# Performance work log

Measured on AMD Instinct MI355X. Metric: run time of the kernel, lower is better.

## Reference

```python
import jax, jax.numpy as jnp
import numpy as np

D_CONV = 4
DT_RANK = 64
D_STATE = 16

def silu(v):
    return v * jax.nn.sigmoid(v)

def setup_inputs() -> dict:
    key = jax.random.key(0)
    ks = jax.random.split(key, 10)
    B, L, d_model, d_inner = 2, 2048, 1024, 2048
    def nrm(k, shape, scale):
        return jax.random.normal(k, shape, dtype=jnp.float32) * scale
    A = jnp.tile(jnp.arange(1, D_STATE + 1, dtype=jnp.float32), (d_inner, 1))
    return {
        'x': nrm(ks[0], (B, L, d_model), 1.0),
        'W_in': nrm(ks[1], (d_model, 2 * d_inner), d_model ** -0.5),
        'conv_w': nrm(ks[2], (d_inner, D_CONV), D_CONV ** -0.5),
        'conv_b': nrm(ks[3], (d_inner,), 0.02),
        'W_x': nrm(ks[4], (d_inner, DT_RANK + 2 * D_STATE), d_inner ** -0.5),
        'W_dt': nrm(ks[5], (DT_RANK, d_inner), DT_RANK ** -0.5),
        'b_dt': nrm(ks[6], (d_inner,), 0.02),
        'A_log': jnp.log(A),
        'D': jnp.ones((d_inner,), dtype=jnp.float32),
        'W_out': nrm(ks[7], (d_inner, d_model), d_inner ** -0.5),
    }

def reference(x, W_in, conv_w, conv_b, W_x, W_dt, b_dt, A_log, D, W_out):
    B, L, _ = x.shape
    d_inner = W_dt.shape[1]
    # input projection and gate split
    xz = x @ W_in                                   # [B, L, 2*d_inner]
    xb, z = jnp.split(xz, 2, axis=-1)
    # causal depthwise conv1d (pad left d_conv-1, then first L outputs)
    xp = jnp.pad(xb, ((0, 0), (D_CONV - 1, 0), (0, 0)))
    xc = sum(xp[:, k:k + L, :] * conv_w[:, k] for k in range(D_CONV)) + conv_b
    xb = silu(xc)                                   # [B, L, d_inner]
    # data-dependent SSM parameters
    x_dbl = xb @ W_x                                # [B, L, dt_rank + 2*d_state]
    dt_low, Bm, Cm = jnp.split(x_dbl, [DT_RANK, DT_RANK + D_STATE], axis=-1)
    dt = jax.nn.softplus(dt_low @ W_dt + b_dt)      # [B, L, d_inner]
    A = -jnp.exp(A_log)                             # [d_inner, d_state]

    def step(h, inp):
        dt_t, B_t, C_t, x_t = inp                   # [B,d_inner],[B,n],[B,n],[B,d_inner]
        dA = jnp.exp(A * dt_t[..., None])           # [B, d_inner, d_state]
        h = h * dA + (x_t * dt_t)[..., None] * B_t[:, None, :]
        y = jnp.einsum('bdn,bn->bd', h, C_t)
        return h, y

    xs = (dt.swapaxes(0, 1), Bm.swapaxes(0, 1), Cm.swapaxes(0, 1), xb.swapaxes(0, 1))
    h0 = jnp.zeros((B, d_inner, D_STATE), dtype=x.dtype)
    _, ys = jax.lax.scan(step, h0, xs)              # ys: [L, B, d_inner]
    y = ys.swapaxes(0, 1) + xb * D
    out = y * silu(z)
    return out @ W_out
```

## Files before the change

kernel.cpp:

```cpp
#include <hip/hip_runtime.h>
#include <hip/hip_bf16.h>


#define BATCH   2
#define SEQLEN  2048
#define DMODEL  1024
#define DINNER  2048
#define DCONV   4
#define DTRANK  64
#define DSTATE  16
#define BL      (BATCH * SEQLEN)
#define NXZ     (2 * DINNER)
#define XDBL_N  (DTRANK + 2 * DSTATE)
#define LCH     32
#define NCHUNK  (SEQLEN / LCH)
#define KSPLIT  8
#define KC      (DINNER / KSPLIT)
#define KS_OUT  4
#define KCO     (DINNER / KS_OUT)
#define KS_XD   8
#define KCX     (DINNER / KS_XD)
#define XDP     128

typedef __bf16 bf16x8 __attribute__((ext_vector_type(8)));
typedef __bf16 bf16x4 __attribute__((ext_vector_type(4)));
typedef float  floatx4 __attribute__((ext_vector_type(4)));

__device__ __forceinline__ float silu_f(float v) {
    return v / (1.f + __expf(-v));
}

__device__ __forceinline__ float softplus_f(float v) {
    return (v > 20.f) ? v : __logf(1.f + __expf(v));
}

__device__ __forceinline__ float fast_exp2(float v) {
    return __builtin_amdgcn_exp2f(v);
}

__device__ __forceinline__ void gload_lds16(const __bf16* g, __bf16* l) {
    __builtin_amdgcn_global_load_lds(
        (const __attribute__((address_space(1))) void*)g,
        (__attribute__((address_space(3))) void*)l, 16, 0, 0);
}

#define VMW(n) asm volatile("s_waitcnt vmcnt(" #n ")" ::: "memory")
#define BARX() __builtin_amdgcn_s_barrier()

template <int BUF, int QA>
__device__ __forceinline__ void rdA(const char* rA, bf16x8 (&aF)[4][2]) {
#pragma unroll
    for (int j = 0; j < 4; ++j) {
        aF[j][0] = *(const bf16x8*)(rA + BUF * 65536 + ((QA * 4 + j) * 2 + 0) * 1024);
        aF[j][1] = *(const bf16x8*)(rA + BUF * 65536 + ((QA * 4 + j) * 2 + 1) * 1024);
    }
}

template <int BUF, int QB>
__device__ __forceinline__ void rdB(const char* rB, bf16x8 (&bF)[2][2]) {
#pragma unroll
    for (int f = 0; f < 2; ++f) {
        bF[f][0] = *(const bf16x8*)(rB + BUF * 65536 + QB * 8192 + f * 2048 + 0);
        bF[f][1] = *(const bf16x8*)(rB + BUF * 65536 + QB * 8192 + f * 2048 + 1024);
    }
}

template <int QA, int QB>
__device__ __forceinline__ void mf16(const bf16x8 (&aF)[4][2], const bf16x8 (&bF)[2][2],
                                     floatx4 (&acc)[8][4]) {
    __builtin_amdgcn_s_setprio(1);
#pragma unroll
    for (int ks = 0; ks < 2; ++ks)
#pragma unroll
        for (int j = 0; j < 4; ++j)
#pragma unroll
            for (int f = 0; f < 2; ++f)
                acc[QA * 4 + j][QB * 2 + f] = __builtin_amdgcn_mfma_f32_16x16x32_bf16(
                    aF[j][ks], bF[f][ks], acc[QA * 4 + j][QB * 2 + f], 0, 0, 0);
    __builtin_amdgcn_s_setprio(0);
}

template <int BUF, int QA>
__device__ __forceinline__ void stA2(const __bf16* gAs, char* sm, int lda, int w, int t) {
    gload_lds16(gAs + (size_t)(QA * 64) * lda + t * 64,
                (__bf16*)(sm + BUF * 65536 + QA * 8192 + w * 1024));
    gload_lds16(gAs + (size_t)(128 + QA * 64) * lda + t * 64,
                (__bf16*)(sm + BUF * 65536 + 16384 + QA * 8192 + w * 1024));
}

template <int BUF, int QB>
__device__ __forceinline__ void stB2(const __bf16* gBs, char* sm, int lda, int w, int t) {
    gload_lds16(gBs + (size_t)(QB * 32) * lda + t * 64,
                (__bf16*)(sm + BUF * 65536 + 32768 + QB * 8192 + w * 1024));
    gload_lds16(gBs + (size_t)(128 + QB * 32) * lda + t * 64,
                (__bf16*)(sm + BUF * 65536 + 32768 + 16384 + QB * 8192 + w * 1024));
}

template <int EPI>
__global__ __launch_bounds__(512, 2) void gemm_bt_256(
    const __bf16* __restrict__ A,
    const __bf16* __restrict__ BT,
    void* __restrict__ Cv,
    int M, int N, int K, int lda,
    const float* __restrict__ bias)
{
    __shared__ __align__(16) char smem[131072];

    const int tid  = threadIdx.x;
    const int w    = tid >> 6;
    const int lane = tid & 63;

    const int cpx = gridDim.x >> 3;
    const int swz = (blockIdx.x & 7) * cpx + (blockIdx.x >> 3);
    const int ntn = N >> 8;
    const int row0 = (swz / ntn) << 8;
    const int col0 = (swz % ntn) << 8;
    const int kbase = blockIdx.y * K;

    const int P     = tid;
    const int rr    = (P >> 2) & 15;
    const int qq    = (P & 3) ^ (2 * ((P >> 5) & 1));
    const int colE  = (((P >> 6) & 1) * 4 + qq) * 8;
    const int rgP   = P >> 7;
    const int rowAu = rgP * 16 + rr;
    const int rowBu = (rgP >> 1) * 64 + (rgP & 1) * 16 + rr;

    const __bf16* gAs = A  + (size_t)(row0 + rowAu) * lda + kbase + colE;
    const __bf16* gBs = BT + (size_t)(col0 + rowBu) * lda + kbase + colE;
    char* sm = smem;

    const int lsw = ((lane & 15) * 4 + ((lane >> 4) ^ (2 * ((lane >> 3) & 1)))) * 16;
    const char* rA = smem + (w >> 2) * 16384 + lsw;
    const char* rB = smem + 32768 + ((w & 3) >> 1) * 16384 + ((w & 3) & 1) * 4096 + lsw;

    floatx4 acc[8][4];
#pragma unroll
    for (int i = 0; i < 8; ++i)
#pragma unroll
        for (int j = 0; j < 4; ++j)
            acc[i][j] = (floatx4){0.f, 0.f, 0.f, 0.f};
    bf16x8 aF[4][2], bF[2][2];

    const int NT = K >> 6;
    const int NI = NT >> 1;

    stA2<0, 0>(gAs, sm, lda, w, 0);
    stB2<0, 0>(gBs, sm, lda, w, 0);
    stB2<0, 1>(gBs, sm, lda, w, 0);
    stA2<0, 1>(gAs, sm, lda, w, 0);
    stA2<1, 0>(gAs, sm, lda, w, 1);
    stB2<1, 1>(gBs, sm, lda, w, 1);
    VMW(6);
    BARX();

    for (int i = 0; i < NI - 1; ++i) {
        const int t1 = 2 * i + 1, t2 = 2 * i + 2, t3 = 2 * i + 3;
        rdA<0, 0>(rA, aF); rdB<0, 0>(rB, bF);
        stB2<1, 0>(gBs, sm, lda, w, t1);
        BARX(); mf16<0, 0>(aF, bF, acc); BARX();
        rdB<0, 1>(rB, bF);
        stA2<1, 1>(gAs, sm, lda, w, t1);
        BARX(); mf16<0, 1>(aF, bF, acc); VMW(8); BARX();
        rdA<0, 1>(rA, aF);
        stA2<0, 0>(gAs, sm, lda, w, t2);
        BARX(); mf16<1, 1>(aF, bF, acc); BARX();
        rdB<0, 0>(rB, bF);
        stB2<0, 1>(gBs, sm, lda, w, t2);
        BARX(); mf16<1, 0>(aF, bF, acc); VMW(6); BARX();
        rdA<1, 0>(rA, aF); rdB<1, 0>(rB, bF);
        stB2<0, 0>(gBs, sm, lda, w, t2);
        BARX(); mf16<0, 0>(aF, bF, acc); BARX();
        rdB<1, 1>(rB, bF);
        stA2<0, 1>(gAs, sm, lda, w, t2);
        BARX(); mf16<0, 1>(aF, bF, acc); VMW(8); BARX();
        rdA<1, 1>(rA, aF);
        stA2<1, 0>(gAs, sm, lda, w, t3);
        BARX(); mf16<1, 1>(aF, bF, acc); BARX();
        rdB<1, 0>(rB, bF);
        stB2<1, 1>(gBs, sm, lda, w, t3);
        BARX(); mf16<1, 0>(aF, bF, acc); VMW(6); BARX();
    }
    {
        const int t1 = NT - 1;
        rdA<0, 0>(rA, aF); rdB<0, 0>(rB, bF);
        stB2<1, 0>(gBs, sm, lda, w, t1);
        BARX(); mf16<0, 0>(aF, bF, acc); BARX();
        rdB<0, 1>(rB, bF);
        stA2<1, 1>(gAs, sm, lda, w, t1);
        BARX(); mf16<0, 1>(aF, bF, acc); VMW(8); BARX();
        rdA<0, 1>(rA, aF);
        BARX(); mf16<1, 1>(aF, bF, acc); BARX();
        rdB<0, 0>(rB, bF);
        BARX(); mf16<1, 0>(aF, bF, acc); VMW(2); BARX();
        rdA<1, 0>(rA, aF); rdB<1, 0>(rB, bF);
        BARX(); mf16<0, 0>(aF, bF, acc); BARX();
        rdB<1, 1>(rB, bF);
        BARX(); mf16<0, 1>(aF, bF, acc); VMW(0); BARX();
        rdA<1, 1>(rA, aF);
        BARX(); mf16<1, 1>(aF, bF, acc); BARX();
        rdB<1, 0>(rB, bF);
        BARX(); mf16<1, 0>(aF, bF, acc);
    }

    const int lrow = lane & 15, quad = lane >> 4;
    const int rbase = row0 + (w >> 2) * 128;
    const int cbase = col0 + (w & 3) * 64;
    const size_t cofs = (size_t)blockIdx.y * (size_t)M * (size_t)N;
#pragma unroll
    for (int fi = 0; fi < 8; ++fi) {
#pragma unroll
        for (int cf = 0; cf < 4; ++cf) {
            const int col = cbase + cf * 16 + lrow;
            const float bv = (EPI == 1 || EPI == 3) ? bias[col] : 0.f;
#pragma unroll
            for (int r = 0; r < 4; ++r) {
                const int row = rbase + fi * 16 + quad * 4 + r;
                float v = acc[fi][cf][r];
                if (EPI == 1 || EPI == 3) v = softplus_f(v + bv);
                if (EPI == 2 || EPI == 3)
                    ((__bf16*)Cv)[(size_t)row * N + col] = (__bf16)v;
                else
                    ((float*)Cv)[cofs + (size_t)row * N + col] = v;
            }
        }
    }
    (void)M;
}

__global__ __launch_bounds__(256) void out_reduce(
    const float* __restrict__ parts, float* __restrict__ out)
{
    const size_t i = ((size_t)blockIdx.x * 256 + threadIdx.x) * 4;
    floatx4 s = *(const floatx4*)(parts + i);
#pragma unroll
    for (int kz = 1; kz < KS_OUT; ++kz)
        s += *(const floatx4*)(parts + (size_t)kz * BL * DMODEL + i);
    *(floatx4*)(out + i) = s;
}

template <int EPI>
__global__ __launch_bounds__(256) void gemm_r64(
    const __bf16* __restrict__ A,
    const __bf16* __restrict__ BT,
    void* __restrict__ Cv,
    int M, int N, int K,
    const float* __restrict__ bias)
{
    __shared__ __bf16 Asm[64 * 32];
    __shared__ __bf16 Bsm[128 * 32];

    const int tid  = threadIdx.x;
    const int w    = tid >> 6;
    const int lane = tid & 63;
    const int lrow = lane & 15;
    const int quad = lane >> 4;
    const int row0 = blockIdx.y * 64;
    const int col0 = blockIdx.x * 128;
    const int wc   = w * 32;

    const int ldr = tid >> 2;
    const int ldk = (tid & 3) * 8;
    const __bf16* gA = A  + (size_t)(row0 + ldr) * K + ldk;
    const __bf16* gB = BT + (size_t)(col0 + ldr) * K + ldk;
    const size_t half = (size_t)64 * K;
    __bf16* lA0 = Asm + w * 512;
    __bf16* lB0 = Bsm + w * 512;
    __bf16* lB1 = Bsm + 2048 + w * 512;

    floatx4 acc[4][2];
#pragma unroll
    for (int i = 0; i < 4; ++i)
#pragma unroll
        for (int j = 0; j < 2; ++j)
            acc[i][j] = (floatx4){0.f, 0.f, 0.f, 0.f};

    for (int k0 = 0; k0 < K; k0 += 32) {
        gload_lds16(gA, lA0);
        gload_lds16(gB, lB0);
        gload_lds16(gB + half, lB1);
        gA += 32; gB += 32;
        __syncthreads();

        bf16x8 af[4], bf[2];
#pragma unroll
        for (int t = 0; t < 4; ++t)
            af[t] = *(const bf16x8*)(Asm + (t * 16 + lrow) * 32 + quad * 8);
#pragma unroll
        for (int u = 0; u < 2; ++u)
            bf[u] = *(const bf16x8*)(Bsm + (wc + u * 16 + lrow) * 32 + quad * 8);

#pragma unroll
        for (int ti = 0; ti < 4; ++ti)
#pragma unroll
            for (int tj = 0; tj < 2; ++tj)
                acc[ti][tj] = __builtin_amdgcn_mfma_f32_16x16x32_bf16(
                    af[ti], bf[tj], acc[ti][tj], 0, 0, 0);
        __syncthreads();
    }

#pragma unroll
    for (int ti = 0; ti < 4; ++ti) {
#pragma unroll
        for (int tj = 0; tj < 2; ++tj) {
            int col = col0 + wc + tj * 16 + lrow;
            float bv = (EPI == 1 || EPI == 3) ? bias[col] : 0.f;
#pragma unroll
            for (int r = 0; r < 4; ++r) {
                int row = row0 + ti * 16 + quad * 4 + r;
                float v = acc[ti][tj][r];
                if (EPI == 1 || EPI == 3) v = softplus_f(v + bv);
                if (EPI == 2 || EPI == 3)
                    ((__bf16*)Cv)[(size_t)row * N + col] = (__bf16)v;
                else
                    ((float*)Cv)[(size_t)row * N + col] = v;
            }
        }
    }
}

__global__ __launch_bounds__(256) void xdbl_gemm(
    const __bf16* __restrict__ A,
    const __bf16* __restrict__ BT,
    float* __restrict__ parts)
{
    __shared__ __bf16 Asm[64 * 32];
    __shared__ __bf16 Bsm[128 * 32];

    const int tid  = threadIdx.x;
    const int w    = tid >> 6;
    const int lane = tid & 63;
    const int lrow = lane & 15;
    const int quad = lane >> 4;
    const int row0 = blockIdx.x * 64;
    const int kbeg = blockIdx.y * KCX;
    const int wc   = w * 32;

    const int ldr = tid >> 2;
    const int ldk = (tid & 3) * 8;
    const __bf16* gA = A  + (size_t)(row0 + ldr) * DINNER + kbeg + ldk;
    const __bf16* gB = BT + (size_t)ldr * DINNER + kbeg + ldk;
    const size_t half = (size_t)64 * DINNER;
    __bf16* lA0 = Asm + w * 512;
    __bf16* lB0 = Bsm + w * 512;
    __bf16* lB1 = Bsm + 2048 + w * 512;

    floatx4 acc[4][2];
#pragma unroll
    for (int i = 0; i < 4; ++i)
#pragma unroll
        for (int j = 0; j < 2; ++j)
            acc[i][j] = (floatx4){0.f, 0.f, 0.f, 0.f};

    for (int k0 = 0; k0 < KCX; k0 += 32) {
        gload_lds16(gA, lA0);
        gload_lds16(gB, lB0);
        gload_lds16(gB + half, lB1);
        gA += 32; gB += 32;
        __syncthreads();

        bf16x8 af[4], bf[2];
#pragma unroll
        for (int t = 0; t < 4; ++t)
            af[t] = *(const bf16x8*)(Asm + (t * 16 + lrow) * 32 + quad * 8);
#pragma unroll
        for (int u = 0; u < 2; ++u)
            bf[u] = *(const bf16x8*)(Bsm + (wc + u * 16 + lrow) * 32 + quad * 8);

#pragma unroll
        for (int ti = 0; ti < 4; ++ti)
#pragma unroll
            for (int tj = 0; tj < 2; ++tj)
                acc[ti][tj] = __builtin_amdgcn_mfma_f32_16x16x32_bf16(
                    af[ti], bf[tj], acc[ti][tj], 0, 0, 0);
        __syncthreads();
    }

    const size_t base = (size_t)blockIdx.y * BL * XDP;
#pragma unroll
    for (int ti = 0; ti < 4; ++ti) {
#pragma unroll
        for (int tj = 0; tj < 2; ++tj) {
            int col = wc + tj * 16 + lrow;
#pragma unroll
            for (int r = 0; r < 4; ++r) {
                int row = row0 + ti * 16 + quad * 4 + r;
                parts[base + (size_t)row * XDP + col] = acc[ti][tj][r];
            }
        }
    }
}

__global__ __launch_bounds__(256) void xdbl_reduce2(
    const float* __restrict__ parts, float* __restrict__ xdbl,
    __bf16* __restrict__ dtlow16)
{
    const int i4  = blockIdx.x * 256 + threadIdx.x;
    const int row = i4 / 24;
    const int c4  = i4 - row * 24;
    const float* p = parts + (size_t)row * XDP + c4 * 4;
    floatx4 s = *(const floatx4*)p;
#pragma unroll
    for (int kz = 1; kz < KS_XD; ++kz)
        s += *(const floatx4*)(p + (size_t)kz * BL * XDP);
    *(floatx4*)(xdbl + (size_t)row * XDBL_N + c4 * 4) = s;
    if (c4 < 16) {
        bf16x4 o = {(__bf16)s.x, (__bf16)s.y, (__bf16)s.z, (__bf16)s.w};
        *(bf16x4*)(dtlow16 + (size_t)row * DTRANK + c4 * 4) = o;
    }
}

#define NB_CAST  ((BL * DMODEL / 4) / 256)
#define NB_WIN   ((NXZ / 32) * (DMODEL / 32))
#define NB_WOUT  ((DMODEL / 32) * (DINNER / 32))
#define NB_WDT   ((DINNER / 32) * (DTRANK / 32))
#define NB_CW    ((DCONV * DINNER) / 256)

__device__ __forceinline__ void transpose_tile(
    const float* __restrict__ src, __bf16* __restrict__ dst, int R, int Cc,
    int bx, int by, int tid, float* tile)
{
    int tx = tid & 31, ty = tid >> 5;
    int c0 = bx * 32, r0 = by * 32;
#pragma unroll
    for (int i = 0; i < 32; i += 8)
        tile[(ty + i) * 33 + tx] = src[(size_t)(r0 + ty + i) * Cc + c0 + tx];
    __syncthreads();
#pragma unroll
    for (int i = 0; i < 32; i += 8)
        dst[(size_t)(c0 + ty + i) * R + r0 + tx] = (__bf16)tile[tx * 33 + ty + i];
}

__global__ __launch_bounds__(256) void prep_kernel(
    const float* __restrict__ x,
    const float* __restrict__ W_in,
    const float* __restrict__ W_out,
    const float* __restrict__ W_dt,
    const float* __restrict__ conv_w,
    __bf16* __restrict__ xb16,
    __bf16* __restrict__ WiT16,
    __bf16* __restrict__ WoT16,
    __bf16* __restrict__ WdtT16,
    float* __restrict__ cwT)
{
    __shared__ float tile[32 * 33];
    const int tid = threadIdx.x;
    int bid = blockIdx.x;

    if (bid < NB_CAST) {
        long i = ((long)bid * 256 + tid) * 4;
        float4 v = *(const float4*)(x + i);
        bf16x4 o = {(__bf16)v.x, (__bf16)v.y, (__bf16)v.z, (__bf16)v.w};
        *(bf16x4*)(xb16 + i) = o;
        return;
    }
    bid -= NB_CAST;
    if (bid < NB_WIN) {
        transpose_tile(W_in, WiT16, DMODEL, NXZ,
                       bid % (NXZ / 32), bid / (NXZ / 32), tid, tile);
        return;
    }
    bid -= NB_WIN;
    if (bid < NB_WOUT) {
        transpose_tile(W_out, WoT16, DINNER, DMODEL,
                       bid % (DMODEL / 32), bid / (DMODEL / 32), tid, tile);
        return;
    }
    bid -= NB_WOUT;
    if (bid < NB_WDT) {
        transpose_tile(W_dt, WdtT16, DTRANK, DINNER,
                       bid % (DINNER / 32), bid / (DINNER / 32), tid, tile);
        return;
    }
    bid -= NB_WDT;
    {
        int i = bid * 256 + tid;
        int k = i / DINNER, d = i % DINNER;
        cwT[i] = conv_w[d * DCONV + k];
    }
}

#define NB_CONV  ((BL / 64) * KSPLIT)
#define NB_WXT   ((DINNER / 32) * (XDBL_N / 32))

__global__ __launch_bounds__(256) void conv_prep(
    const __bf16* __restrict__ xz16,
    const float* __restrict__ cwT,
    const float* __restrict__ cb,
    const float* __restrict__ W_x,
    __bf16* __restrict__ xc16,
    __bf16* __restrict__ WxT16)
{
    __shared__ float tile[32 * 33];
    const int tid = threadIdx.x;
    const int bid = blockIdx.x;

    if (bid >= NB_CONV) {
        const int b2 = bid - NB_CONV;
        transpose_tile(W_x, WxT16, DINNER, XDBL_N,
                       b2 % (XDBL_N / 32), b2 / (XDBL_N / 32), tid, tile);
        return;
    }

    const int row0 = (bid >> 3) * 64;
    const int kbeg = (bid & 7) * KC;
    const int ct = (tid & 31) * 8;
    const int rt = (tid >> 5) * 8;
    const int d  = kbeg + ct;

    float wreg[DCONV][8];
#pragma unroll
    for (int k = 0; k < DCONV; ++k) {
        float4 a = *(const float4*)(cwT + k * DINNER + d);
        float4 b = *(const float4*)(cwT + k * DINNER + d + 4);
        wreg[k][0]=a.x; wreg[k][1]=a.y; wreg[k][2]=a.z; wreg[k][3]=a.w;
        wreg[k][4]=b.x; wreg[k][5]=b.y; wreg[k][6]=b.z; wreg[k][7]=b.w;
    }
    float bias8[8];
    {
        float4 a = *(const float4*)(cb + d);
        float4 b = *(const float4*)(cb + d + 4);
        bias8[0]=a.x; bias8[1]=a.y; bias8[2]=a.z; bias8[3]=a.w;
        bias8[4]=b.x; bias8[5]=b.y; bias8[6]=b.z; bias8[7]=b.w;
    }

    const bf16x8 zero = {};
    bf16x8 win[DCONV];
    const int tloc0 = (int)((row0 + rt) & (SEQLEN - 1));
#pragma unroll
    for (int j = 0; j < DCONV - 1; ++j)
        win[j] = (tloc0 - 3 + j >= 0)
            ? *(const bf16x8*)(xz16 + (size_t)(row0 + rt - 3 + j) * NXZ + d)
            : zero;

    for (int i = 0; i < 8; ++i) {
        size_t r = (size_t)row0 + rt + i;
        win[DCONV - 1] = *(const bf16x8*)(xz16 + r * NXZ + d);
        bf16x8 o;
#pragma unroll
        for (int j = 0; j < 8; ++j) {
            float acc = bias8[j];
#pragma unroll
            for (int k = 0; k < DCONV; ++k)
                acc += (float)win[k][j] * wreg[k][j];
            o[j] = (__bf16)silu_f(acc);
        }
        *(bf16x8*)(xc16 + r * DINNER + d) = o;
#pragma unroll
        for (int k = 0; k < DCONV - 1; ++k)
            win[k] = win[k + 1];
    }
}

__global__ __launch_bounds__(256) void scan_pass1(
    const __bf16* __restrict__ dt16,
    const __bf16* __restrict__ xc16,
    const float* __restrict__ xdbl,
    const float* __restrict__ A_log,
    float* __restrict__ sums_h,
    float* __restrict__ sums_p)
{
    const int d  = blockIdx.x * 256 + threadIdx.x;
    const int bc = blockIdx.y;
    const int b  = bc / NCHUNK, c = bc % NCHUNK;
    const long r0 = (long)b * SEQLEN + (long)c * LCH;

    float Ad[DSTATE];
    {
        const float4* al = (const float4*)(A_log + d * DSTATE);
#pragma unroll
        for (int q = 0; q < 4; ++q) {
            float4 v = al[q];
            Ad[q * 4 + 0] = -__expf(v.x) * 1.44269504f;
            Ad[q * 4 + 1] = -__expf(v.y) * 1.44269504f;
            Ad[q * 4 + 2] = -__expf(v.z) * 1.44269504f;
            Ad[q * 4 + 3] = -__expf(v.w) * 1.44269504f;
        }
    }

    float h[DSTATE] = {};
    float Pp[DSTATE];
#pragma unroll
    for (int n = 0; n < DSTATE; ++n) Pp[n] = 1.f;

    for (int t = 0; t < LCH; ++t) {
        long r = r0 + t;
        float dtv = (float)dt16[r * DINNER + d];
        float xv  = (float)xc16[r * DINNER + d];
        float xdt = xv * dtv;
        const float4* bv = (const float4*)(xdbl + r * XDBL_N + DTRANK);
        float4 B0 = bv[0], B1 = bv[1], B2 = bv[2], B3 = bv[3];
        const float Bn[DSTATE] = {B0.x,B0.y,B0.z,B0.w, B1.x,B1.y,B1.z,B1.w,
                                  B2.x,B2.y,B2.z,B2.w, B3.x,B3.y,B3.z,B3.w};
#pragma unroll
        for (int n = 0; n < DSTATE; ++n) {
            float dA = fast_exp2(Ad[n] * dtv);
            h[n] = h[n] * dA + xdt * Bn[n];
            Pp[n] *= dA;
        }
    }

    const long rowbase = (long)bc * DSTATE;
#pragma unroll
    for (int n = 0; n < DSTATE; ++n) {
        sums_h[(rowbase + n) * DINNER + d] = h[n];
        sums_p[(rowbase + n) * DINNER + d] = Pp[n];
    }
}

__global__ __launch_bounds__(256) void scan_combine(
    float* __restrict__ sums_h, float* __restrict__ sums_p)
{
    int u = blockIdx.x * 256 + threadIdx.x;
    int d = u & (DINNER - 1);
    int n = (u >> 11) & (DSTATE - 1);
    int b = u >> 15;
    float hg = 0.f;
    for (int c = 0; c < NCHUNK; ++c) {
        long row = (long)(b * NCHUNK + c) * DSTATE + n;
        float p  = sums_p[row * DINNER + d];
        float hl = sums_h[row * DINNER + d];
        sums_p[row * DINNER + d] = hg;
        hg = p * hg + hl;
    }
}

__global__ __launch_bounds__(256) void scan_pass3(
    const __bf16* __restrict__ dt16,
    const __bf16* __restrict__ xc16,
    const float* __restrict__ xdbl,
    const float* __restrict__ A_log,
    const __bf16* __restrict__ xz16,
    const float* __restrict__ sums_p,
    const float* __restrict__ Dp,
    __bf16* __restrict__ gated)
{
    const int d  = blockIdx.x * 256 + threadIdx.x;
    const int bc = blockIdx.y;
    const int b  = bc / NCHUNK, c = bc % NCHUNK;
    const long r0 = (long)b * SEQLEN + (long)c * LCH;

    float Ad[DSTATE];
    {
        const float4* al = (const float4*)(A_log + d * DSTATE);
#pragma unroll
        for (int q = 0; q < 4; ++q) {
            float4 v = al[q];
            Ad[q * 4 + 0] = -__expf(v.x) * 1.44269504f;
            Ad[q * 4 + 1] = -__expf(v.y) * 1.44269504f;
            Ad[q * 4 + 2] = -__expf(v.z) * 1.44269504f;
            Ad[q * 4 + 3] = -__expf(v.w) * 1.44269504f;
        }
    }

    float h[DSTATE];
    const long rowbase = (long)bc * DSTATE;
#pragma unroll
    for (int n = 0; n < DSTATE; ++n)
        h[n] = sums_p[(rowbase + n) * DINNER + d];

    const float Dv = Dp[d];

    for (int t = 0; t < LCH; ++t) {
        long r = r0 + t;
        float dtv = (float)dt16[r * DINNER + d];
        float xv  = (float)xc16[r * DINNER + d];
        float xdt = xv * dtv;
        const float4* bv = (const float4*)(xdbl + r * XDBL_N + DTRANK);
        float4 B0 = bv[0], B1 = bv[1], B2 = bv[2], B3 = bv[3];
        float4 C0 = bv[4], C1 = bv[5], C2 = bv[6], C3 = bv[7];
        const float Bn[DSTATE] = {B0.x,B0.y,B0.z,B0.w, B1.x,B1.y,B1.z,B1.w,
                                  B2.x,B2.y,B2.z,B2.w, B3.x,B3.y,B3.z,B3.w};
        const float Cn[DSTATE] = {C0.x,C0.y,C0.z,C0.w, C1.x,C1.y,C1.z,C1.w,
                                  C2.x,C2.y,C2.z,C2.w, C3.x,C3.y,C3.z,C3.w};
        float y = 0.f;
#pragma unroll
        for (int n = 0; n < DSTATE; ++n) {
            float dA = fast_exp2(Ad[n] * dtv);
            h[n] = h[n] * dA + xdt * Bn[n];
            y += h[n] * Cn[n];
        }
        float z = (float)xz16[r * NXZ + DINNER + d];
        float yy = y + xv * Dv;
        gated[r * DINNER + d] = (__bf16)(yy * silu_f(z));
    }
}

extern "C" void kernel_launch(void* const* d_in, const int* in_sizes, int n_in,
                              void* d_out, int out_size, void* d_ws, size_t ws_size,
                              hipStream_t stream) {
    const float* x      = (const float*)d_in[0];
    const float* W_in   = (const float*)d_in[1];
    const float* conv_w = (const float*)d_in[2];
    const float* conv_b = (const float*)d_in[3];
    const float* W_x    = (const float*)d_in[4];
    const float* W_dt   = (const float*)d_in[5];
    const float* b_dt   = (const float*)d_in[6];
    const float* A_log  = (const float*)d_in[7];
    const float* Dp     = (const float*)d_in[8];
    const float* W_out  = (const float*)d_in[9];
    float* out = (float*)d_out;

    __bf16* xz16    = (__bf16*)d_ws;
    __bf16* xc16    = xz16 + (long)BL * NXZ;
    __bf16* dt16    = xc16 + (long)BL * DINNER;
    __bf16* gated16 = dt16 + (long)BL * DINNER;
    __bf16* WoT16   = gated16 + (long)BL * DINNER;
    __bf16* WdtT16  = WoT16 + (long)DINNER * DMODEL;
    __bf16* dtlow16 = WdtT16 + (long)DINNER * DTRANK;
    __bf16* xb16    = dtlow16 + (long)BL * DTRANK;
    __bf16* WiT16   = xb16 + (long)BL * DMODEL;
    float*  xdbl    = (float*)(WiT16 + (long)NXZ * DMODEL);
    float*  cwT     = xdbl + (long)BL * XDBL_N;
    float*  scratch = cwT + (long)DCONV * DINNER;
    float*  sums_h  = scratch;
    float*  sums_p  = scratch + (long)BATCH * NCHUNK * DSTATE * DINNER;
    __bf16* WxT16 = xb16;
    float* outparts = (float*)d_ws;

    dim3 blk(256);

    prep_kernel<<<dim3(NB_CAST + NB_WIN + NB_WOUT + NB_WDT + NB_CW), blk, 0, stream>>>(
        x, W_in, W_out, W_dt, conv_w, xb16, WiT16, WoT16, WdtT16, cwT);

    gemm_bt_256<2><<<dim3((BL / 256) * (NXZ / 256)), dim3(512), 0, stream>>>(
        xb16, WiT16, xz16, BL, NXZ, DMODEL, DMODEL, nullptr);

    conv_prep<<<dim3(NB_CONV + NB_WXT), blk, 0, stream>>>(
        xz16, cwT, conv_b, W_x, xc16, WxT16);

    xdbl_gemm<<<dim3(BL / 64, KS_XD), blk, 0, stream>>>(xc16, WxT16, scratch);
    xdbl_reduce2<<<dim3((BL * 24) / 256), blk, 0, stream>>>(scratch, xdbl, dtlow16);

    gemm_r64<3><<<dim3(DINNER / 128, BL / 64), blk, 0, stream>>>(
        dtlow16, WdtT16, dt16, BL, DINNER, DTRANK, b_dt);

    {
        dim3 grid1(DINNER / 256, BATCH * NCHUNK);
        scan_pass1<<<grid1, blk, 0, stream>>>(dt16, xc16, xdbl, A_log, sums_h, sums_p);
        scan_combine<<<dim3((BATCH * DSTATE * DINNER) / 256), blk, 0, stream>>>(
            sums_h, sums_p);
        scan_pass3<<<grid1, blk, 0, stream>>>(dt16, xc16, xdbl, A_log, xz16,
                                              sums_p, Dp, gated16);
    }
    gemm_bt_256<0><<<dim3((BL / 256) * (DMODEL / 256), KS_OUT), dim3(512), 0, stream>>>(
        gated16, WoT16, outparts, BL, DMODEL, KCO, DINNER, nullptr);
    out_reduce<<<dim3((BL * DMODEL) / 1024), blk, 0, stream>>>(outparts, out);

    (void)in_sizes; (void)n_in; (void)out_size; (void)ws_size;
}
```

Measured before the change: 278.7 us.

## Store dt and conv output time-major per channel for vectorized scan loads

The dt GEMM epilogue now writes dt transposed as [d][t], and the conv kernel also writes a transposed copy of its output. The scan passes can then read 8 consecutive timesteps per thread with one 16-byte load instead of strided scalar loads. Pass 1 now computes the chunk decay product as exp2(A*sum(dt)) instead of multiplying 16 running products, which removes multiplies but changes rounding slightly. WxT is moved to the sums_p scratch to make room, and the transposed stores use a column-strided write pattern.

```diff
diff --git a/kernel.cpp b/kernel.cpp
--- a/kernel.cpp
+++ b/kernel.cpp
@@ -303,16 +303,25 @@
 #pragma unroll
         for (int tj = 0; tj < 2; ++tj) {
             int col = col0 + wc + tj * 16 + lrow;
-            float bv = (EPI == 1 || EPI == 3) ? bias[col] : 0.f;
-#pragma unroll
-            for (int r = 0; r < 4; ++r) {
-                int row = row0 + ti * 16 + quad * 4 + r;
-                float v = acc[ti][tj][r];
-                if (EPI == 1 || EPI == 3) v = softplus_f(v + bv);
-                if (EPI == 2 || EPI == 3)
-                    ((__bf16*)Cv)[(size_t)row * N + col] = (__bf16)v;
-                else
-                    ((float*)Cv)[(size_t)row * N + col] = v;
+            float bv = (EPI == 1 || EPI == 3 || EPI == 4) ? bias[col] : 0.f;
+            if (EPI == 4) {
+                bf16x4 ov;
+#pragma unroll
+                for (int r = 0; r < 4; ++r)
+                    ov[r] = (__bf16)softplus_f(acc[ti][tj][r] + bv);
+                int rowb = row0 + ti * 16 + quad * 4;
+                *(bf16x4*)((__bf16*)Cv + (size_t)col * M + rowb) = ov;
+            } else {
+#pragma unroll
+                for (int r = 0; r < 4; ++r) {
+                    int row = row0 + ti * 16 + quad * 4 + r;
+                    float v = acc[ti][tj][r];
+                    if (EPI == 1 || EPI == 3) v = softplus_f(v + bv);
+                    if (EPI == 2 || EPI == 3)
+                        ((__bf16*)Cv)[(size_t)row * N + col] = (__bf16)v;
+                    else
+                        ((float*)Cv)[(size_t)row * N + col] = v;
+                }
             }
         }
     }
@@ -488,6 +497,7 @@
     const float* __restrict__ cb,
     const float* __restrict__ W_x,
     __bf16* __restrict__ xc16,
+    __bf16* __restrict__ xcT16,
     __bf16* __restrict__ WxT16)
 {
     __shared__ float tile[32 * 33];
@@ -525,6 +535,7 @@
 
     const bf16x8 zero = {};
     bf16x8 win[DCONV];
+    bf16x8 oT[8];
     const int tloc0 = (int)((row0 + rt) & (SEQLEN - 1));
 #pragma unroll
     for (int j = 0; j < DCONV - 1; ++j)
@@ -546,14 +557,19 @@
         }
         *(bf16x8*)(xc16 + r * DINNER + d) = o;
 #pragma unroll
+        for (int j = 0; j < 8; ++j) oT[j][i] = o[j];
+#pragma unroll
         for (int k = 0; k < DCONV - 1; ++k)
             win[k] = win[k + 1];
     }
+#pragma unroll
+    for (int j = 0; j < 8; ++j)
+        *(bf16x8*)(xcT16 + (size_t)(d + j) * BL + row0 + rt) = oT[j];
 }
 
 __global__ __launch_bounds__(256) void scan_pass1(
-    const __bf16* __restrict__ dt16,
-    const __bf16* __restrict__ xc16,
+    const __bf16* __restrict__ dtT,
+    const __bf16* __restrict__ xcT,
     const float* __restrict__ xdbl,
     const float* __restrict__ A_log,
     float* __restrict__ sums_h,
@@ -578,24 +594,28 @@
     }
 
     float h[DSTATE] = {};
-    float Pp[DSTATE];
-#pragma unroll
-    for (int n = 0; n < DSTATE; ++n) Pp[n] = 1.f;
-
-    for (int t = 0; t < LCH; ++t) {
-        long r = r0 + t;
-        float dtv = (float)dt16[r * DINNER + d];
-        float xv  = (float)xc16[r * DINNER + d];
-        float xdt = xv * dtv;
-        const float4* bv = (const float4*)(xdbl + r * XDBL_N + DTRANK);
-        float4 B0 = bv[0], B1 = bv[1], B2 = bv[2], B3 = bv[3];
-        const float Bn[DSTATE] = {B0.x,B0.y,B0.z,B0.w, B1.x,B1.y,B1.z,B1.w,
-                                  B2.x,B2.y,B2.z,B2.w, B3.x,B3.y,B3.z,B3.w};
-#pragma unroll
-        for (int n = 0; n < DSTATE; ++n) {
-            float dA = fast_exp2(Ad[n] * dtv);
-            h[n] = h[n] * dA + xdt * Bn[n];
-            Pp[n] *= dA;
+    float Sdt = 0.f;
+    const __bf16* pdt = dtT + (size_t)d * BL + r0;
+    const __bf16* pxc = xcT + (size_t)d * BL + r0;
+    const float*  pB  = xdbl + (size_t)r0 * XDBL_N + DTRANK;
+
+    for (int g = 0; g < LCH / 8; ++g) {
+        bf16x8 dt8 = *(const bf16x8*)(pdt + g * 8);
+        bf16x8 xv8 = *(const bf16x8*)(pxc + g * 8);
+#pragma unroll
+        for (int u = 0; u < 8; ++u) {
+            float dtv = (float)dt8[u];
+            float xdt = (float)xv8[u] * dtv;
+            Sdt += dtv;
+            const float4* bv = (const float4*)(pB + (g * 8 + u) * XDBL_N);
+            float4 B0 = bv[0], B1 = bv[1], B2 = bv[2], B3 = bv[3];
+            const float Bn[DSTATE] = {B0.x,B0.y,B0.z,B0.w, B1.x,B1.y,B1.z,B1.w,
+                                      B2.x,B2.y,B2.z,B2.w, B3.x,B3.y,B3.z,B3.w};
+#pragma unroll
+            for (int n = 0; n < DSTATE; ++n) {
+                float dA = fast_exp2(Ad[n] * dtv);
+                h[n] = h[n] * dA + xdt * Bn[n];
+            }
         }
     }
 
@@ -603,7 +623,7 @@
 #pragma unroll
     for (int n = 0; n < DSTATE; ++n) {
         sums_h[(rowbase + n) * DINNER + d] = h[n];
-        sums_p[(rowbase + n) * DINNER + d] = Pp[n];
+        sums_p[(rowbase + n) * DINNER + d] = fast_exp2(Ad[n] * Sdt);
     }
 }
 
@@ -625,8 +645,8 @@
 }
 
 __global__ __launch_bounds__(256) void scan_pass3(
-    const __bf16* __restrict__ dt16,
-    const __bf16* __restrict__ xc16,
+    const __bf16* __restrict__ dtT,
+    const __bf16* __restrict__ xcT,
     const float* __restrict__ xdbl,
     const float* __restrict__ A_log,
     const __bf16* __restrict__ xz16,
@@ -659,29 +679,38 @@
         h[n] = sums_p[(rowbase + n) * DINNER + d];
 
     const float Dv = Dp[d];
-
-    for (int t = 0; t < LCH; ++t) {
-        long r = r0 + t;
-        float dtv = (float)dt16[r * DINNER + d];
-        float xv  = (float)xc16[r * DINNER + d];
-        float xdt = xv * dtv;
-        const float4* bv = (const float4*)(xdbl + r * XDBL_N + DTRANK);
-        float4 B0 = bv[0], B1 = bv[1], B2 = bv[2], B3 = bv[3];
-        float4 C0 = bv[4], C1 = bv[5], C2 = bv[6], C3 = bv[7];
-        const float Bn[DSTATE] = {B0.x,B0.y,B0.z,B0.w, B1.x,B1.y,B1.z,B1.w,
-                                  B2.x,B2.y,B2.z,B2.w, B3.x,B3.y,B3.z,B3.w};
-        const float Cn[DSTATE] = {C0.x,C0.y,C0.z,C0.w, C1.x,C1.y,C1.z,C1.w,
-                                  C2.x,C2.y,C2.z,C2.w, C3.x,C3.y,C3.z,C3.w};
-        float y = 0.f;
-#pragma unroll
-        for (int n = 0; n < DSTATE; ++n) {
-            float dA = fast_exp2(Ad[n] * dtv);
-            h[n] = h[n] * dA + xdt * Bn[n];
-            y += h[n] * Cn[n];
+    const __bf16* pdt = dtT + (size_t)d * BL + r0;
+    const __bf16* pxc = xcT + (size_t)d * BL + r0;
+    const float*  pBC = xdbl + (size_t)r0 * XDBL_N + DTRANK;
+    const __bf16* pz  = xz16 + (size_t)r0 * NXZ + DINNER + d;
+    __bf16*       pg  = gated + (size_t)r0 * DINNER + d;
+
+    for (int g = 0; g < LCH / 8; ++g) {
+        bf16x8 dt8 = *(const bf16x8*)(pdt + g * 8);
+        bf16x8 xv8 = *(const bf16x8*)(pxc + g * 8);
+#pragma unroll
+        for (int u = 0; u < 8; ++u) {
+            float dtv = (float)dt8[u];
+            float xv  = (float)xv8[u];
+            float xdt = xv * dtv;
+            const float4* bv = (const float4*)(pBC + (g * 8 + u) * XDBL_N);
+            float4 B0 = bv[0], B1 = bv[1], B2 = bv[2], B3 = bv[3];
+            float4 C0 = bv[4], C1 = bv[5], C2 = bv[6], C3 = bv[7];
+            const float Bn[DSTATE] = {B0.x,B0.y,B0.z,B0.w, B1.x,B1.y,B1.z,B1.w,
+                                      B2.x,B2.y,B2.z,B2.w, B3.x,B3.y,B3.z,B3.w};
+            const float Cn[DSTATE] = {C0.x,C0.y,C0.z,C0.w, C1.x,C1.y,C1.z,C1.w,
+                                      C2.x,C2.y,C2.z,C2.w, C3.x,C3.y,C3.z,C3.w};
+            float y = 0.f;
+#pragma unroll
+            for (int n = 0; n < DSTATE; ++n) {
+                float dA = fast_exp2(Ad[n] * dtv);
+                h[n] = h[n] * dA + xdt * Bn[n];
+                y += h[n] * Cn[n];
+            }
+            float z = (float)pz[(size_t)(g * 8 + u) * NXZ];
+            float yy = y + xv * Dv;
+            pg[(size_t)(g * 8 + u) * DINNER] = (__bf16)(yy * silu_f(z));
         }
-        float z = (float)xz16[r * NXZ + DINNER + d];
-        float yy = y + xv * Dv;
-        gated[r * DINNER + d] = (__bf16)(yy * silu_f(z));
     }
 }
 
@@ -702,8 +731,8 @@
 
     __bf16* xz16    = (__bf16*)d_ws;
     __bf16* xc16    = xz16 + (long)BL * NXZ;
-    __bf16* dt16    = xc16 + (long)BL * DINNER;
-    __bf16* gated16 = dt16 + (long)BL * DINNER;
+    __bf16* dtT16   = xc16 + (long)BL * DINNER;
+    __bf16* gated16 = dtT16 + (long)BL * DINNER;
     __bf16* WoT16   = gated16 + (long)BL * DINNER;
     __bf16* WdtT16  = WoT16 + (long)DINNER * DMODEL;
     __bf16* dtlow16 = WdtT16 + (long)DINNER * DTRANK;
@@ -714,7 +743,8 @@
     float*  scratch = cwT + (long)DCONV * DINNER;
     float*  sums_h  = scratch;
     float*  sums_p  = scratch + (long)BATCH * NCHUNK * DSTATE * DINNER;
-    __bf16* WxT16 = xb16;
+    __bf16* xcT16 = xb16;
+    __bf16* WxT16 = (__bf16*)sums_p;
     float* outparts = (float*)d_ws;
 
     dim3 blk(256);
@@ -726,20 +756,21 @@
         xb16, WiT16, xz16, BL, NXZ, DMODEL, DMODEL, nullptr);
 
     conv_prep<<<dim3(NB_CONV + NB_WXT), blk, 0, stream>>>(
-        xz16, cwT, conv_b, W_x, xc16, WxT16);
+        xz16, cwT, conv_b, W_x, xc16, xcT16, WxT16);
 
     xdbl_gemm<<<dim3(BL / 64, KS_XD), blk, 0, stream>>>(xc16, WxT16, scratch);
     xdbl_reduce2<<<dim3((BL * 24) / 256), blk, 0, stream>>>(scratch, xdbl, dtlow16);
 
-    gemm_r64<3><<<dim3(DINNER / 128, BL / 64), blk, 0, stream>>>(
-        dtlow16, WdtT16, dt16, BL, DINNER, DTRANK, b_dt);
+    gemm_r64<4><<<dim3(DINNER / 128, BL / 64), blk, 0, stream>>>(
+        dtlow16, WdtT16, dtT16, BL, DINNER, DTRANK, b_dt);
 
     {
         dim3 grid1(DINNER / 256, BATCH * NCHUNK);
-        scan_pass1<<<grid1, blk, 0, stream>>>(dt16, xc16, xdbl, A_log, sums_h, sums_p);
+        scan_pass1<<<grid1, blk, 0, stream>>>(dtT16, xcT16, xdbl, A_log,
+                                              sums_h, sums_p);
         scan_combine<<<dim3((BATCH * DSTATE * DINNER) / 256), blk, 0, stream>>>(
             sums_h, sums_p);
-        scan_pass3<<<grid1, blk, 0, stream>>>(dt16, xc16, xdbl, A_log, xz16,
+        scan_pass3<<<grid1, blk, 0, stream>>>(dtT16, xcT16, xdbl, A_log, xz16,
                                               sums_p, Dp, gated16);
     }
     gemm_bt_256<0><<<dim3((BL / 256) * (DMODEL / 256), KS_OUT), dim3(512), 0, stream>>>(
```

Measured after the change: 286.1 us. 2.7% more time.

## Stage bf16 GEMM epilogue through swizzled LDS and compute chunk decay from summed dt

Applied to the files above, without the earlier changes.

For bf16-output GEMM epilogues, accumulator values are first written into a XOR-swizzled shared-memory tile and then stored to global memory as 16-byte vectors, replacing scattered 2-byte stores. Separately, the chunk-scan kernel stops multiplying a running per-state decay product and instead accumulates the sum of dt, computing the chunk decay once as exp2(A*sum(dt)). The first change aims to cut the number of global store transactions, at the cost of two block barriers and LDS reuse. The second removes 16 multiplies per timestep but changes rounding slightly.

```diff
diff --git a/kernel.cpp b/kernel.cpp
--- a/kernel.cpp
+++ b/kernel.cpp
@@ -203,24 +203,51 @@
     }
 
     const int lrow = lane & 15, quad = lane >> 4;
-    const int rbase = row0 + (w >> 2) * 128;
-    const int cbase = col0 + (w & 3) * 64;
-    const size_t cofs = (size_t)blockIdx.y * (size_t)M * (size_t)N;
-#pragma unroll
-    for (int fi = 0; fi < 8; ++fi) {
-#pragma unroll
-        for (int cf = 0; cf < 4; ++cf) {
-            const int col = cbase + cf * 16 + lrow;
-            const float bv = (EPI == 1 || EPI == 3) ? bias[col] : 0.f;
-#pragma unroll
-            for (int r = 0; r < 4; ++r) {
-                const int row = rbase + fi * 16 + quad * 4 + r;
-                float v = acc[fi][cf][r];
-                if (EPI == 1 || EPI == 3) v = softplus_f(v + bv);
-                if (EPI == 2 || EPI == 3)
-                    ((__bf16*)Cv)[(size_t)row * N + col] = (__bf16)v;
-                else
+
+    if (EPI == 2 || EPI == 3) {
+        __syncthreads();
+#pragma unroll
+        for (int fi = 0; fi < 8; ++fi) {
+#pragma unroll
+            for (int cf = 0; cf < 4; ++cf) {
+                const int lc = (w & 3) * 64 + cf * 16 + lrow;
+                const float bv = (EPI == 3) ? bias[col0 + lc] : 0.f;
+#pragma unroll
+                for (int r = 0; r < 4; ++r) {
+                    const int lr = (w >> 2) * 128 + fi * 16 + quad * 4 + r;
+                    float v = acc[fi][cf][r];
+                    if (EPI == 3) v = softplus_f(v + bv);
+                    const int ck = (lc >> 3) ^ ((lr >> 2) & 7);
+                    *(__bf16*)(smem + lr * 512 + ck * 16 + (lc & 7) * 2) = (__bf16)v;
+                }
+            }
+        }
+        __syncthreads();
+#pragma unroll
+        for (int it = 0; it < 16; ++it) {
+            const int row = it * 16 + w * 2 + (lane >> 5);
+            const int cr  = lane & 31;
+            const int ck  = cr ^ ((row >> 2) & 7);
+            bf16x8 v = *(const bf16x8*)(smem + row * 512 + ck * 16);
+            *(bf16x8*)((__bf16*)Cv + (size_t)(row0 + row) * N + col0 + cr * 8) = v;
+        }
+    } else {
+        const size_t cofs = (size_t)blockIdx.y * (size_t)M * (size_t)N;
+        const int rbase = row0 + (w >> 2) * 128;
+        const int cbase = col0 + (w & 3) * 64;
+#pragma unroll
+        for (int fi = 0; fi < 8; ++fi) {
+#pragma unroll
+            for (int cf = 0; cf < 4; ++cf) {
+                const int col = cbase + cf * 16 + lrow;
+                const float bv = (EPI == 1) ? bias[col] : 0.f;
+#pragma unroll
+                for (int r = 0; r < 4; ++r) {
+                    const int row = rbase + fi * 16 + quad * 4 + r;
+                    float v = acc[fi][cf][r];
+                    if (EPI == 1) v = softplus_f(v + bv);
                     ((float*)Cv)[cofs + (size_t)row * N + col] = v;
+                }
             }
         }
     }
@@ -578,15 +605,14 @@
     }
 
     float h[DSTATE] = {};
-    float Pp[DSTATE];
-#pragma unroll
-    for (int n = 0; n < DSTATE; ++n) Pp[n] = 1.f;
+    float Sdt = 0.f;
 
     for (int t = 0; t < LCH; ++t) {
         long r = r0 + t;
         float dtv = (float)dt16[r * DINNER + d];
         float xv  = (float)xc16[r * DINNER + d];
         float xdt = xv * dtv;
+        Sdt += dtv;
         const float4* bv = (const float4*)(xdbl + r * XDBL_N + DTRANK);
         float4 B0 = bv[0], B1 = bv[1], B2 = bv[2], B3 = bv[3];
         const float Bn[DSTATE] = {B0.x,B0.y,B0.z,B0.w, B1.x,B1.y,B1.z,B1.w,
@@ -595,7 +621,6 @@
         for (int n = 0; n < DSTATE; ++n) {
             float dA = fast_exp2(Ad[n] * dtv);
             h[n] = h[n] * dA + xdt * Bn[n];
-            Pp[n] *= dA;
         }
     }
 
@@ -603,7 +628,7 @@
 #pragma unroll
     for (int n = 0; n < DSTATE; ++n) {
         sums_h[(rowbase + n) * DINNER + d] = h[n];
-        sums_p[(rowbase + n) * DINNER + d] = Pp[n];
+        sums_p[(rowbase + n) * DINNER + d] = fast_exp2(Ad[n] * Sdt);
     }
 }
 
```

Measured after the change: 280.9 us. Within noise of the previous version (+0.8%).
